# Kernel tuning notes

Measured on AMD Instinct MI355X. Metric: run time of the kernel, lower is better.

Reference implementation:

```python
import jax, jax.numpy as jnp
import numpy as np

B, D, C, Q = 4096, 128, 1000, 65536
PROTO_M = 0.99
EPS = 1e-12


def _l2norm(x, axis=-1):
    n = jnp.sqrt(jnp.sum(x * x, axis=axis, keepdims=True))
    return x / jnp.maximum(n, EPS)


def setup_inputs() -> dict:
    key = jax.random.key(0)
    ks = jax.random.split(key, 7)
    q = _l2norm(jax.random.normal(ks[0], (B, D), dtype=jnp.float32))
    k = _l2norm(jax.random.normal(ks[1], (B, D), dtype=jnp.float32))
    classfy_logits = jax.random.normal(ks[2], (B, C), dtype=jnp.float32)
    plabel = jax.random.uniform(ks[3], (B, C), dtype=jnp.float32)
    prototypes = _l2norm(jax.random.normal(ks[4], (C, D), dtype=jnp.float32))
    queue = _l2norm(jax.random.normal(ks[5], (Q, D), dtype=jnp.float32))
    queue_pseudo = jax.random.randint(ks[6], (Q,), 0, C).astype(jnp.float32)
    return {
        "q": q, "k": k, "classfy_logits": classfy_logits, "plabel": plabel,
        "prototypes": prototypes, "queue": queue, "queue_pseudo": queue_pseudo,
        "ptr": 0,
    }


def reference(q, k, classfy_logits, plabel, prototypes, queue, queue_pseudo, ptr):
    m = PROTO_M
    # classifier softmax (encoder head output)
    classfy_out = jax.nn.softmax(classfy_logits, axis=1)          # [B, C]
    # cluster logits against OLD prototypes (mm happens before EMA update)
    logits_prot = jnp.matmul(q, prototypes.T)                     # [B, C]
    cluster_out = jax.nn.softmax(logits_prot, axis=1)
    # pseudo labels from partial-label-masked scores
    pseudo_labels = jnp.argmax(classfy_out * plabel, axis=1)      # [B] int
    # --- vectorized order-dependent scatter-EMA prototype update ---
    # sequential: proto[l_i] = m*proto[l_i] + (1-m)*q_i  for i = 0..B-1
    # closed form: proto[c]*m^{n_c} + sum_i (1-m)*m^{(#later samples with same label)} q_i
    onehot = (pseudo_labels[:, None] == jnp.arange(C)[None, :])   # [B, C] bool
    counts = jnp.sum(onehot, axis=0)                              # [C] n_c
    rank = jnp.take_along_axis(jnp.cumsum(onehot.astype(jnp.int32), axis=0),
                               pseudo_labels[:, None], axis=1)[:, 0] - 1  # [B]
    n_l = counts[pseudo_labels]                                   # [B]
    w = (1.0 - m) * jnp.power(jnp.float32(m), (n_l - 1 - rank).astype(jnp.float32))
    scatter = jnp.zeros_like(prototypes).at[pseudo_labels].add(w[:, None] * q)
    decay = jnp.power(jnp.float32(m), counts.astype(jnp.float32))[:, None]
    new_prototypes = _l2norm(prototypes * decay + scatter, axis=1)
    # --- MoCo queue enqueue/dequeue (contrastive bank uses OLD queue) ---
    cont_features = jnp.concatenate([q, k, queue], axis=0)        # [2B+Q, D]
    pl_f = pseudo_labels.astype(jnp.float32)
    cont_labels = jnp.concatenate([pl_f, pl_f, queue_pseudo], axis=0)
    new_queue = jax.lax.dynamic_update_slice(queue, k, (ptr, 0))
    new_queue_pseudo = jax.lax.dynamic_update_slice(queue_pseudo, pl_f, (ptr,))
    new_ptr = (ptr + q.shape[0]) % queue.shape[0]
    return (classfy_out, cluster_out, cont_features, cont_labels,
            new_prototypes, new_queue, new_queue_pseudo, new_ptr)
```

## Files before the change

### kernel.cpp

```cpp
#include <hip/hip_runtime.h>
#include <hip/hip_bf16.h>
#include <math.h>

#define Bn 4096
#define Dn 128
#define Cn 1000
#define Qn 65536
#define CPAD 1024

typedef __attribute__((ext_vector_type(8))) short short8v;
typedef __attribute__((ext_vector_type(4))) short short4v;
typedef __attribute__((ext_vector_type(4))) float f32x4;
typedef __attribute__((ext_vector_type(4))) float f4v;

__device__ inline float waveAllMaxF(float v) {
    for (int o = 32; o; o >>= 1) v = fmaxf(v, __shfl_xor(v, o));
    return v;
}
__device__ inline float waveAllSumF(float v) {
    for (int o = 32; o; o >>= 1) v += __shfl_xor(v, o);
    return v;
}
__device__ inline float waveSumF(float v) {
    for (int o = 32; o; o >>= 1) v += __shfl_down(v, o);
    return v;
}
__device__ inline short f2bf(float x) {
    union { __hip_bfloat16 h; short s; } u;
    u.h = __float2bfloat16(x);
    return u.s;
}

__global__ __launch_bounds__(256) void k_cls(
    const float* __restrict__ logits, const float* __restrict__ plabel,
    const float* __restrict__ q, const float* __restrict__ proto,
    float* __restrict__ out_cls, int* __restrict__ labels,
    __hip_bfloat16* __restrict__ qb, __hip_bfloat16* __restrict__ pb)
{
    int g = blockIdx.x, t = threadIdx.x;

    if (t < 160) {
        int idx4 = g * 160 + t;
        if (idx4 < 131072) {
            f4v v = *(const f4v*)(q + (long long)idx4 * 4);
            short4v o = {f2bf(v.x), f2bf(v.y), f2bf(v.z), f2bf(v.w)};
            *(short4v*)((short*)qb + (long long)idx4 * 4) = o;
        } else {
            int j4 = idx4 - 131072;
            short4v o = {0, 0, 0, 0};
            if (j4 < 32000) {
                f4v v = *(const f4v*)(proto + (long long)j4 * 4);
                o = (short4v){f2bf(v.x), f2bf(v.y), f2bf(v.z), f2bf(v.w)};
            }
            *(short4v*)((short*)pb + (long long)j4 * 4) = o;
        }
    }

    int lane = t & 63, wid = t >> 6;
    int row = g * 4 + wid;
    const float* x = logits + (long long)row * Cn;

    float vv[16];
    float mx = -INFINITY;
#pragma unroll
    for (int j = 0; j < 4; ++j) {
        int f4i = lane + j * 64;
        f4v v = (f4v){-INFINITY, -INFINITY, -INFINITY, -INFINITY};
        if (f4i < 250) v = *(const f4v*)(x + f4i * 4);
        vv[j * 4 + 0] = v.x; vv[j * 4 + 1] = v.y;
        vv[j * 4 + 2] = v.z; vv[j * 4 + 3] = v.w;
        mx = fmaxf(mx, fmaxf(fmaxf(v.x, v.y), fmaxf(v.z, v.w)));
    }
    mx = waveAllMaxF(mx);

    float ssum = 0.f;
#pragma unroll
    for (int u = 0; u < 16; ++u) {
        vv[u] = expf(vv[u] - mx);
        ssum += vv[u];
    }
    ssum = waveAllSumF(ssum);
    float inv = 1.f / ssum;

    float bv = -INFINITY; int bi = Cn;
#pragma unroll
    for (int j = 0; j < 4; ++j) {
        int f4i = lane + j * 64;
        if (f4i < 250) {
            float o0 = vv[j * 4 + 0] * inv, o1 = vv[j * 4 + 1] * inv;
            float o2 = vv[j * 4 + 2] * inv, o3 = vv[j * 4 + 3] * inv;
            *((f4v*)(out_cls + (long long)row * Cn) + f4i) = (f4v){o0, o1, o2, o3};
            f4v p4 = *((const f4v*)(plabel + (long long)row * Cn) + f4i);
            float pr[4] = {o0 * p4.x, o1 * p4.y, o2 * p4.z, o3 * p4.w};
#pragma unroll
            for (int jj = 0; jj < 4; ++jj) {
                if (pr[jj] > bv) { bv = pr[jj]; bi = f4i * 4 + jj; }
            }
        }
    }
    for (int o = 32; o; o >>= 1) {
        float ov = __shfl_xor(bv, o);
        int   oi = __shfl_xor(bi, o);
        if (ov > bv || (ov == bv && oi < bi)) { bv = ov; bi = oi; }
    }
    if (lane == 0) labels[row] = bi;
}

__global__ __launch_bounds__(256) void k_rest(
    const __hip_bfloat16* __restrict__ qb, const __hip_bfloat16* __restrict__ pb,
    const float* __restrict__ proto, const float* __restrict__ q,
    const float* __restrict__ kk, const float* __restrict__ queue,
    const int* __restrict__ lbl, const float* __restrict__ qps,
    const int* __restrict__ ptrp,
    float* __restrict__ outC, float* __restrict__ outp,
    float* __restrict__ out_lab, float* __restrict__ out_qps,
    float* __restrict__ out_ptr,
    float* __restrict__ out_feat, float* __restrict__ out_queue)
{
    __shared__ __align__(16) char smem[32800];
    int bid = blockIdx.x, t = threadIdx.x;

    if (bid >= 1301) {
        int cidx = bid - 1301;
        int p = *ptrp;
        int pc = p < 0 ? 0 : (p > Qn - Bn ? Qn - Bn : p);
        const long long QD = (long long)Bn * Dn;
        const long long n4 = (2 * QD + (long long)Qn * Dn) / 4;
        const long long stride = 2048LL * 256;
        for (long long i = (long long)cidx * 256 + t; i < n4; i += stride) {
            long long off = i * 4;
            if (off < QD) {
                *(f4v*)(out_feat + off) = *(const f4v*)(q + off);
            } else if (off < 2 * QD) {
                *(f4v*)(out_feat + off) = *(const f4v*)(kk + off - QD);
            } else {
                long long qoff = off - 2 * QD;
                f4v v = *(const f4v*)(queue + qoff);
                *(f4v*)(out_feat + off) = v;
                int row = (int)(qoff >> 7);
                int col = (int)(qoff & 127);
                unsigned rr = (unsigned)(row - pc);
                if (rr < (unsigned)Bn) v = *(const f4v*)(kk + (long long)rr * Dn + col);
                *(f4v*)(out_queue + qoff) = v;
            }
        }
        return;
    }

    if (bid < 256) {
        float (*red)[4] = (float (*)[4])smem;
        int lane = t & 63, w = t >> 6;
        int la = lane & 15, lk = lane >> 4;
        int row0 = bid * 16;

        f32x4 acc[16];
#pragma unroll
        for (int j = 0; j < 16; ++j) acc[j] = (f32x4){0.f, 0.f, 0.f, 0.f};

        const short* A = (const short*)qb + (long long)(row0 + la) * Dn;
        const short* Bp = (const short*)pb;
#pragma unroll
        for (int kc = 0; kc < Dn; kc += 32) {
            short8v a = *(const short8v*)(A + kc + lk * 8);
#pragma unroll
            for (int j = 0; j < 16; ++j) {
                int prow = w * 256 + j * 16 + la;
                short8v b = *(const short8v*)(Bp + (long long)prow * Dn + kc + lk * 8);
                acc[j] = __builtin_amdgcn_mfma_f32_16x16x32_bf16(a, b, acc[j], 0, 0, 0);
            }
        }

        float m[4];
#pragma unroll
        for (int rg = 0; rg < 4; ++rg) {
            float v = -INFINITY;
#pragma unroll
            for (int j = 0; j < 16; ++j) {
                int col = w * 256 + j * 16 + la;
                if (col < Cn) v = fmaxf(v, acc[j][rg]);
            }
#pragma unroll
            for (int o = 1; o < 16; o <<= 1) v = fmaxf(v, __shfl_xor(v, o));
            m[rg] = v;
        }
        if (la == 0) {
#pragma unroll
            for (int rg = 0; rg < 4; ++rg) red[lk * 4 + rg][w] = m[rg];
        }
        __syncthreads();
#pragma unroll
        for (int rg = 0; rg < 4; ++rg) {
            int r = lk * 4 + rg;
            m[rg] = fmaxf(fmaxf(red[r][0], red[r][1]), fmaxf(red[r][2], red[r][3]));
        }
        __syncthreads();

        float s[4];
#pragma unroll
        for (int rg = 0; rg < 4; ++rg) {
            float v = 0.f;
#pragma unroll
            for (int j = 0; j < 16; ++j) {
                int col = w * 256 + j * 16 + la;
                float e = (col < Cn) ? expf(acc[j][rg] - m[rg]) : 0.f;
                acc[j][rg] = e;
                v += e;
            }
#pragma unroll
            for (int o = 1; o < 16; o <<= 1) v += __shfl_xor(v, o);
            s[rg] = v;
        }
        if (la == 0) {
#pragma unroll
            for (int rg = 0; rg < 4; ++rg) red[lk * 4 + rg][w] = s[rg];
        }
        __syncthreads();
#pragma unroll
        for (int rg = 0; rg < 4; ++rg) {
            int r = lk * 4 + rg;
            s[rg] = 1.f / (red[r][0] + red[r][1] + red[r][2] + red[r][3]);
        }

#pragma unroll
        for (int j = 0; j < 16; ++j) {
            int col = w * 256 + j * 16 + la;
            if (col < Cn) {
                int rowb = row0 + lk * 4;
#pragma unroll
                for (int rg = 0; rg < 4; ++rg)
                    outC[(long long)(rowb + rg) * Cn + col] = acc[j][rg] * s[rg];
            }
        }
    } else if (bid < 756) {
        int* sl = (int*)smem;
        unsigned short* list0 = (unsigned short*)(smem + 16384);
        unsigned short* list1 = list0 + 4096;
        int* nm = (int*)(smem + 32768);
        float* shh = (float*)(smem + 32776);

        int h = t >> 7, tt = t & 127;
        int c = (bid - 256) * 2 + h;

#pragma unroll
        for (int u = 0; u < 4; ++u) {
            int base = (u * 256 + t) * 4;
            *(int4*)(sl + base) = *(const int4*)(lbl + base);
        }
        if (t == 0)   nm[0] = 0;
        if (t == 128) nm[1] = 0;
        __syncthreads();

        int wv = t >> 6;
        if ((wv & 1) == 0) {
            int hh = wv >> 1;
            int ln = t & 63;
            int cc = (bid - 256) * 2 + hh;
            unsigned short* lst = hh ? list1 : list0;
            int n = 0;
            for (int jj = 0; jj < Bn / 64; ++jj) {
                unsigned long long mask = __ballot(sl[jj * 64 + ln] == cc);
                if (ln == 0) {
                    while (mask) {
                        int b = __builtin_ctzll(mask);
                        lst[n++] = (unsigned short)(jj * 64 + b);
                        mask &= mask - 1;
                    }
                }
            }
            if (ln == 0) nm[hh] = n;
        }
        __syncthreads();

        int n = nm[h];
        unsigned short* lst = h ? list1 : list0;
        float acc = proto[(long long)c * Dn + tt];
        for (int mi = 0; mi < n; ++mi)
            acc = 0.99f * acc + 0.01f * q[(long long)lst[mi] * Dn + tt];

        float ss = waveSumF(acc * acc);
        if ((t & 63) == 0) shh[t >> 6] = ss;
        __syncthreads();
        float nn = sqrtf(shh[h * 2] + shh[h * 2 + 1]);
        outp[(long long)c * Dn + tt] = acc / fmaxf(nn, 1e-12f);
    } else {
        int gid = (bid - 756) * 256 + t;
        const int NL = 2 * Bn + Qn;
        int p = *ptrp;
        int pc = p < 0 ? 0 : (p > Qn - Bn ? Qn - Bn : p);
        if (gid < NL) {
            float v;
            if (gid < Bn)          v = (float)lbl[gid];
            else if (gid < 2 * Bn) v = (float)lbl[gid - Bn];
            else                   v = qps[gid - 2 * Bn];
            out_lab[gid] = v;
        }
        int j = gid - NL;
        if (j >= 0 && j < Qn) {
            unsigned rr = (unsigned)(j - pc);
            out_qps[j] = (rr < (unsigned)Bn) ? (float)lbl[rr] : qps[j];
        }
        if (gid == NL + Qn) out_ptr[0] = (float)((p + Bn) % Qn);
    }
}

extern "C" void kernel_launch(void* const* d_in, const int* in_sizes, int n_in,
                              void* d_out, int out_size, void* d_ws, size_t ws_size,
                              hipStream_t stream)
{
    const float* q     = (const float*)d_in[0];
    const float* kk    = (const float*)d_in[1];
    const float* cl    = (const float*)d_in[2];
    const float* plab  = (const float*)d_in[3];
    const float* proto = (const float*)d_in[4];
    const float* queue = (const float*)d_in[5];
    const float* qps   = (const float*)d_in[6];
    const int*   ptrp  = (const int*)d_in[7];

    float* out = (float*)d_out;
    const long long O_CLU  = 4096000;
    const long long O_FEAT = 8192000;
    const long long O_LAB  = 17629184;
    const long long O_PROT = 17702912;
    const long long O_QUE  = 17830912;
    const long long O_QPS  = 26219520;
    const long long O_PTR  = 26285056;

    char* ws = (char*)d_ws;
    int*   lbl = (int*)(ws + 0);
    __hip_bfloat16* qb = (__hip_bfloat16*)(ws + 1048576);
    __hip_bfloat16* pb = (__hip_bfloat16*)(ws + 2097152);

    k_cls<<<1024, 256, 0, stream>>>(cl, plab, q, proto, out, lbl, qb, pb);
    k_rest<<<3349, 256, 0, stream>>>(qb, pb, proto, q, kk, queue, lbl, qps, ptrp,
                                     out + O_CLU, out + O_PROT,
                                     out + O_LAB, out + O_QPS, out + O_PTR,
                                     out + O_FEAT, out + O_QUE);
}
```

Baseline: 47.29 us.

## Restructure copy blocks, hoist plabel loads, parallelize prototype EMA chain

The k_cls kernel now loads plabel alongside the logits up front, so both global loads are in flight together. In k_rest, the grid-stride copy loop becomes one block per 4096-element chunk, and the copy blocks are placed first in the grid, ahead of the GEMM and prototype blocks. The prototype EMA recurrence is rewritten in closed form, with per-sample power weights replacing the serial multiply dependency, and the loop is unrolled. In exchange it adds more blocks and some __powf cost, with small floating-point differences from the reordered accumulation.

Measured after the change: 51.85 us. 1.1x slower.

```diff
diff --git a/kernel.cpp b/kernel.cpp
--- a/kernel.cpp
+++ b/kernel.cpp
@@ -6,7 +6,6 @@
 #define Dn 128
 #define Cn 1000
 #define Qn 65536
-#define CPAD 1024
 
 typedef __attribute__((ext_vector_type(8))) short short8v;
 typedef __attribute__((ext_vector_type(4))) short short4v;
@@ -58,26 +57,37 @@
 
     int lane = t & 63, wid = t >> 6;
     int row = g * 4 + wid;
-    const float* x = logits + (long long)row * Cn;
-
-    float vv[16];
-    float mx = -INFINITY;
+    const float* x  = logits + (long long)row * Cn;
+    const float* pl = plabel + (long long)row * Cn;
+
+    f4v lv[4], pv[4];
 #pragma unroll
     for (int j = 0; j < 4; ++j) {
         int f4i = lane + j * 64;
-        f4v v = (f4v){-INFINITY, -INFINITY, -INFINITY, -INFINITY};
-        if (f4i < 250) v = *(const f4v*)(x + f4i * 4);
-        vv[j * 4 + 0] = v.x; vv[j * 4 + 1] = v.y;
-        vv[j * 4 + 2] = v.z; vv[j * 4 + 3] = v.w;
-        mx = fmaxf(mx, fmaxf(fmaxf(v.x, v.y), fmaxf(v.z, v.w)));
-    }
+        if (f4i < 250) {
+            lv[j] = *(const f4v*)(x + f4i * 4);
+            pv[j] = *(const f4v*)(pl + f4i * 4);
+        } else {
+            lv[j] = (f4v){-INFINITY, -INFINITY, -INFINITY, -INFINITY};
+            pv[j] = (f4v){0.f, 0.f, 0.f, 0.f};
+        }
+    }
+
+    float mx = -INFINITY;
+#pragma unroll
+    for (int j = 0; j < 4; ++j)
+        mx = fmaxf(mx, fmaxf(fmaxf(lv[j].x, lv[j].y), fmaxf(lv[j].z, lv[j].w)));
     mx = waveAllMaxF(mx);
 
+    float vv[16];
     float ssum = 0.f;
 #pragma unroll
-    for (int u = 0; u < 16; ++u) {
-        vv[u] = expf(vv[u] - mx);
-        ssum += vv[u];
+    for (int j = 0; j < 4; ++j) {
+        vv[j * 4 + 0] = expf(lv[j].x - mx);
+        vv[j * 4 + 1] = expf(lv[j].y - mx);
+        vv[j * 4 + 2] = expf(lv[j].z - mx);
+        vv[j * 4 + 3] = expf(lv[j].w - mx);
+        ssum += vv[j * 4 + 0] + vv[j * 4 + 1] + vv[j * 4 + 2] + vv[j * 4 + 3];
     }
     ssum = waveAllSumF(ssum);
     float inv = 1.f / ssum;
@@ -90,8 +100,7 @@
             float o0 = vv[j * 4 + 0] * inv, o1 = vv[j * 4 + 1] * inv;
             float o2 = vv[j * 4 + 2] * inv, o3 = vv[j * 4 + 3] * inv;
             *((f4v*)(out_cls + (long long)row * Cn) + f4i) = (f4v){o0, o1, o2, o3};
-            f4v p4 = *((const f4v*)(plabel + (long long)row * Cn) + f4i);
-            float pr[4] = {o0 * p4.x, o1 * p4.y, o2 * p4.z, o3 * p4.w};
+            float pr[4] = {o0 * pv[j].x, o1 * pv[j].y, o2 * pv[j].z, o3 * pv[j].w};
 #pragma unroll
             for (int jj = 0; jj < 4; ++jj) {
                 if (pr[jj] > bv) { bv = pr[jj]; bi = f4i * 4 + jj; }
@@ -107,7 +116,7 @@
 }
 
 __global__ __launch_bounds__(256) void k_rest(
-    const __hip_bfloat16* __restrict__ qb, const __hip_bfloat16* __restrict__ pb,
+    const __hip_bfloat16* __restrict__ qb, const __hip_bfloat16* __restrict__ pbuf,
     const float* __restrict__ proto, const float* __restrict__ q,
     const float* __restrict__ kk, const float* __restrict__ queue,
     const int* __restrict__ lbl, const float* __restrict__ qps,
@@ -120,45 +129,57 @@
     __shared__ __align__(16) char smem[32800];
     int bid = blockIdx.x, t = threadIdx.x;
 
-    if (bid >= 1301) {
-        int cidx = bid - 1301;
+    if (bid < 256) {
+        const float* src = (bid < 128) ? q : kk;
+        long long sb = (long long)(bid & 127) * 4096;
+        long long db = (long long)bid * 4096;
+        f4v v[4];
+#pragma unroll
+        for (int u = 0; u < 4; ++u)
+            v[u] = *(const f4v*)(src + sb + (u * 256 + t) * 4);
+#pragma unroll
+        for (int u = 0; u < 4; ++u)
+            *(f4v*)(out_feat + db + (u * 256 + t) * 4) = v[u];
+        return;
+    }
+    if (bid < 2304) {
+        int cb = bid - 256;
         int p = *ptrp;
         int pc = p < 0 ? 0 : (p > Qn - Bn ? Qn - Bn : p);
-        const long long QD = (long long)Bn * Dn;
-        const long long n4 = (2 * QD + (long long)Qn * Dn) / 4;
-        const long long stride = 2048LL * 256;
-        for (long long i = (long long)cidx * 256 + t; i < n4; i += stride) {
-            long long off = i * 4;
-            if (off < QD) {
-                *(f4v*)(out_feat + off) = *(const f4v*)(q + off);
-            } else if (off < 2 * QD) {
-                *(f4v*)(out_feat + off) = *(const f4v*)(kk + off - QD);
-            } else {
-                long long qoff = off - 2 * QD;
-                f4v v = *(const f4v*)(queue + qoff);
-                *(f4v*)(out_feat + off) = v;
-                int row = (int)(qoff >> 7);
-                int col = (int)(qoff & 127);
-                unsigned rr = (unsigned)(row - pc);
-                if (rr < (unsigned)Bn) v = *(const f4v*)(kk + (long long)rr * Dn + col);
-                *(f4v*)(out_queue + qoff) = v;
-            }
+        long long base = (long long)cb * 4096;
+        const long long FB = 2LL * Bn * Dn;
+        f4v v[4];
+#pragma unroll
+        for (int u = 0; u < 4; ++u)
+            v[u] = *(const f4v*)(queue + base + (u * 256 + t) * 4);
+#pragma unroll
+        for (int u = 0; u < 4; ++u)
+            *(f4v*)(out_feat + FB + base + (u * 256 + t) * 4) = v[u];
+#pragma unroll
+        for (int u = 0; u < 4; ++u) {
+            long long foff = base + (u * 256 + t) * 4;
+            int row = (int)(foff >> 7);
+            unsigned rr = (unsigned)(row - pc);
+            f4v w = v[u];
+            if (rr < (unsigned)Bn) w = *(const f4v*)(kk + (long long)rr * Dn + (foff & 127));
+            *(f4v*)(out_queue + foff) = w;
         }
         return;
     }
 
-    if (bid < 256) {
+    if (bid < 2560) {
+        int gb = bid - 2304;
         float (*red)[4] = (float (*)[4])smem;
         int lane = t & 63, w = t >> 6;
         int la = lane & 15, lk = lane >> 4;
-        int row0 = bid * 16;
+        int row0 = gb * 16;
 
         f32x4 acc[16];
 #pragma unroll
         for (int j = 0; j < 16; ++j) acc[j] = (f32x4){0.f, 0.f, 0.f, 0.f};
 
         const short* A = (const short*)qb + (long long)(row0 + la) * Dn;
-        const short* Bp = (const short*)pb;
+        const short* Bp = (const short*)pbuf;
 #pragma unroll
         for (int kc = 0; kc < Dn; kc += 32) {
             short8v a = *(const short8v*)(A + kc + lk * 8);
@@ -231,7 +252,7 @@
                     outC[(long long)(rowb + rg) * Cn + col] = acc[j][rg] * s[rg];
             }
         }
-    } else if (bid < 756) {
+    } else if (bid < 3060) {
         int* sl = (int*)smem;
         unsigned short* list0 = (unsigned short*)(smem + 16384);
         unsigned short* list1 = list0 + 4096;
@@ -239,7 +260,7 @@
         float* shh = (float*)(smem + 32776);
 
         int h = t >> 7, tt = t & 127;
-        int c = (bid - 256) * 2 + h;
+        int c = (bid - 2560) * 2 + h;
 
 #pragma unroll
         for (int u = 0; u < 4; ++u) {
@@ -254,7 +275,7 @@
         if ((wv & 1) == 0) {
             int hh = wv >> 1;
             int ln = t & 63;
-            int cc = (bid - 256) * 2 + hh;
+            int cc = (bid - 2560) * 2 + hh;
             unsigned short* lst = hh ? list1 : list0;
             int n = 0;
             for (int jj = 0; jj < Bn / 64; ++jj) {
@@ -273,9 +294,10 @@
 
         int n = nm[h];
         unsigned short* lst = h ? list1 : list0;
-        float acc = proto[(long long)c * Dn + tt];
+        float acc = proto[(long long)c * Dn + tt] * __powf(0.99f, (float)n);
+#pragma unroll 4
         for (int mi = 0; mi < n; ++mi)
-            acc = 0.99f * acc + 0.01f * q[(long long)lst[mi] * Dn + tt];
+            acc += 0.01f * __powf(0.99f, (float)(n - 1 - mi)) * q[(long long)lst[mi] * Dn + tt];
 
         float ss = waveSumF(acc * acc);
         if ((t & 63) == 0) shh[t >> 6] = ss;
@@ -283,7 +305,7 @@
         float nn = sqrtf(shh[h * 2] + shh[h * 2 + 1]);
         outp[(long long)c * Dn + tt] = acc / fmaxf(nn, 1e-12f);
     } else {
-        int gid = (bid - 756) * 256 + t;
+        int gid = (bid - 3060) * 256 + t;
         const int NL = 2 * Bn + Qn;
         int p = *ptrp;
         int pc = p < 0 ? 0 : (p > Qn - Bn ? Qn - Bn : p);
@@ -331,7 +353,7 @@
     __hip_bfloat16* pb = (__hip_bfloat16*)(ws + 2097152);
 
     k_cls<<<1024, 256, 0, stream>>>(cl, plab, q, proto, out, lbl, qb, pb);
-    k_rest<<<3349, 256, 0, stream>>>(qb, pb, proto, q, kk, queue, lbl, qps, ptrp,
+    k_rest<<<3605, 256, 0, stream>>>(qb, pb, proto, q, kk, queue, lbl, qps, ptrp,
                                      out + O_CLU, out + O_PROT,
                                      out + O_LAB, out + O_QPS, out + O_PTR,
                                      out + O_FEAT, out + O_QUE);
```
